# Kernel tuning notes

Measured on AMD Instinct MI355X. Metric: run time of the kernel, lower is better.

Reference implementation:

```python
import jax, jax.numpy as jnp
import numpy as np

T, F, H = 2048, 256, 384  # seq_len, input_size, hidden_size


def setup_inputs() -> dict:
    key = jax.random.key(0)
    ks = jax.random.split(key, 16)
    s = 1.0 / np.sqrt(F)
    d = {"x": jax.random.normal(ks[0], (T, F), jnp.float32)}
    names = ["q", "k", "v", "i", "f", "o"]
    for j, n in enumerate(names):
        d[f"W{n}"] = jax.random.uniform(ks[1 + j], (H, F), jnp.float32, -s, s)
        d[f"b{n}"] = jax.random.uniform(ks[7 + j], (H,), jnp.float32, -s, s)
    d["conv_w"] = jax.random.uniform(ks[13], (1, 1, 4), jnp.float32, -0.5, 0.5)
    d["conv_b"] = jax.random.uniform(ks[14], (1,), jnp.float32, -0.5, 0.5)
    return d


def _forward(x, Wq, bq, Wk, bk, Wv, bv, Wi, bi, Wf, bf, Wo, bo, conv_w, conv_b):
    # Conv1d(1->1, kernel=4, padding=(3,3)) along time, per input feature.
    xt = x.T[:, None, :]  # (F, 1, T)  feature axis acts as batch
    y = jax.lax.conv_general_dilated(xt, conv_w, (1,), [(3, 3)])  # (F, 1, T+3)
    xp = (y[:, 0, :] + conv_b[0]).T  # (T+3, F)

    inv_sqrt_h = 1.0 / jnp.sqrt(jnp.asarray(H, xp.dtype))
    # Precompute all per-step projections with dense GEMMs (time-parallel part).
    q = xp @ Wq.T + bq                      # (T+3, H)
    k = (xp @ Wk.T + bk) * inv_sqrt_h       # (T+3, H); extra bias_k is zero-init
    v = xp @ Wv.T + bv
    i = jnp.exp(xp @ Wi.T + bi)
    f = jax.nn.sigmoid(xp @ Wf.T + bf)
    o = jax.nn.sigmoid(xp @ Wo.T + bo)

    def step(carry, inp):
        C, n = carry                         # C: (H,H), n: (H,)
        qt, kt, vt, it, ft, ot = inp
        C = ft * C + it * jnp.outer(vt, kt)  # broadcast over last axis, as original
        n = ft * n + it * kt
        den = jnp.maximum(jnp.abs(jnp.dot(n, qt)), 1.0)
        h = ot * (C @ qt) / den
        return (C, n), h

    init = (jnp.zeros((H, H), xp.dtype), jnp.zeros((H,), xp.dtype))
    _, hs = jax.lax.scan(step, init, (q, k, v, i, f, o))
    return hs[-1]  # return_all=False -> last hidden state, shape (H,)


def reference(x, Wq, bq, Wk, bk, Wv, bv, Wi, bi, Wf, bf, Wo, bo, conv_w, conv_b):
    return _forward(x, Wq, bq, Wk, bk, Wv, bv, Wi, bi, Wf, bf, Wo, bo, conv_w, conv_b)
```

## Files before the change

kernel.cpp:

```cpp
#include <hip/hip_runtime.h>
#include <math.h>

#define T_IN 2048
#define TP   2051
#define F    256
#define H    384
#define BK   16
#define BT2  32
#define NT2  65
#define NCS  257
#define NC3  257

__device__ __forceinline__ float logsig(float z) {
    return (z >= 0.0f) ? -log1pf(__expf(-z)) : z - log1pf(__expf(z));
}

union F4 { float4 v; float f[4]; };

__global__ __launch_bounds__(256) void k1_front(const float* __restrict__ x,
        const float* __restrict__ cw, const float* __restrict__ cb,
        const float* __restrict__ Wq, const float* __restrict__ bq,
        const float* __restrict__ Wo, const float* __restrict__ bo,
        float* __restrict__ xp, float* __restrict__ q, float* __restrict__ o,
        float* __restrict__ zf) {
    int bid = blockIdx.x;
    int tid = threadIdx.x;
    if (bid < 513) {
        int t = bid * 4 + (tid >> 6);
        int f4 = tid & 63;
        if (t >= TP) return;
        float w[4] = {cw[0], cw[1], cw[2], cw[3]};
        float b = cb[0];
        float4 acc = {b, b, b, b};
        int i0 = t - 3;
        const float4* x4 = (const float4*)x;
        #pragma unroll
        for (int j = 0; j < 4; ++j) {
            int tt = i0 + j;
            if (tt >= 0 && tt < T_IN) {
                float4 xv = x4[tt * 64 + f4];
                acc.x = fmaf(w[j], xv.x, acc.x);
                acc.y = fmaf(w[j], xv.y, acc.y);
                acc.z = fmaf(w[j], xv.z, acc.z);
                acc.w = fmaf(w[j], xv.w, acc.w);
            }
        }
        ((float4*)xp)[t * 64 + f4] = acc;
    } else if (bid < 609) {
        int lane = tid & 63;
        int row = (bid - 513) * 4 + (tid >> 6);
        float w0 = cw[0], b = cb[0];
        float4 xr = ((const float4*)x)[2047 * 64 + lane];
        float4 xv;
        xv.x = fmaf(w0, xr.x, b);
        xv.y = fmaf(w0, xr.y, b);
        xv.z = fmaf(w0, xr.z, b);
        xv.w = fmaf(w0, xr.w, b);
        float4 q4 = *(const float4*)&Wq[row * 256 + lane * 4];
        float4 o4 = *(const float4*)&Wo[row * 256 + lane * 4];
        float aq = fmaf(xv.x, q4.x, fmaf(xv.y, q4.y, fmaf(xv.z, q4.z, xv.w * q4.w)));
        float ao = fmaf(xv.x, o4.x, fmaf(xv.y, o4.y, fmaf(xv.z, o4.z, xv.w * o4.w)));
        #pragma unroll
        for (int off = 32; off; off >>= 1) {
            aq += __shfl_down(aq, off, 64);
            ao += __shfl_down(ao, off, 64);
        }
        if (lane == 0) {
            q[row] = aq + bq[row];
            o[row] = 1.0f / (1.0f + __expf(-(ao + bo[row])));
        }
    } else {
        for (int i = tid; i < 272; i += 256) zf[i] = 0.0f;
    }
}

__global__ __launch_bounds__(256) void k2_proj(
    const float* __restrict__ xp,
    const float* __restrict__ Wk, const float* __restrict__ bk,
    const float* __restrict__ Wi, const float* __restrict__ bi,
    const float* __restrict__ Wf, const float* __restrict__ bf,
    float* __restrict__ zk, float* __restrict__ ai, float* __restrict__ lf,
    float* __restrict__ cs) {
    __shared__ float alds[2][BT2][20];
    __shared__ float wlds[2][BK][66];
    __shared__ float csred[8][66];
    int tid = threadIdx.x;
    int mz = blockIdx.z;
    const float* __restrict__ W    = (mz == 0) ? Wk : (mz == 1) ? Wi : Wf;
    const float* __restrict__ bias = (mz == 0) ? bk : (mz == 1) ? bi : bf;
    int t0 = blockIdx.x * BT2, b0 = blockIdx.y * 64;
    int tx = tid & 31, ty = tid >> 5;
    float2 acc[4];
    #pragma unroll
    for (int u = 0; u < 4; ++u) { acc[u].x = 0.f; acc[u].y = 0.f; }

    int wrow = tid >> 2;
    int wk4 = (tid & 3) * 4;
    int grow = (b0 + wrow) * 256 + wk4;
    int atq = tid >> 2;
    int arow = (t0 + atq) * 256 + wk4;
    bool aval = (tid < 128) && (t0 + atq < TP);

    float4 aw = {0.f, 0.f, 0.f, 0.f};
    float4 ww;
    if (aval) aw = *(const float4*)&xp[arow];
    ww = *(const float4*)&W[grow];

    for (int i = 0; i < 16; ++i) {
        int buf = i & 1;
        if (tid < 128) *(float4*)&alds[buf][atq][wk4] = aw;
        {
            F4 wu; wu.v = ww;
            #pragma unroll
            for (int j = 0; j < 4; ++j)
                wlds[buf][wk4 + j][wrow] = wu.f[j];
        }
        __syncthreads();
        if (i < 15) {
            int k0 = (i + 1) * BK;
            if (aval) aw = *(const float4*)&xp[arow + k0];
            ww = *(const float4*)&W[grow + k0];
        }
        #pragma unroll
        for (int g = 0; g < 4; ++g) {
            F4 av0, av1, av2, av3;
            av0.v = *(const float4*)&alds[buf][4 * ty + 0][4 * g];
            av1.v = *(const float4*)&alds[buf][4 * ty + 1][4 * g];
            av2.v = *(const float4*)&alds[buf][4 * ty + 2][4 * g];
            av3.v = *(const float4*)&alds[buf][4 * ty + 3][4 * g];
            #pragma unroll
            for (int j = 0; j < 4; ++j) {
                float2 w0 = *(const float2*)&wlds[buf][4 * g + j][2 * tx];
                acc[0].x = fmaf(av0.f[j], w0.x, acc[0].x);
                acc[0].y = fmaf(av0.f[j], w0.y, acc[0].y);
                acc[1].x = fmaf(av1.f[j], w0.x, acc[1].x);
                acc[1].y = fmaf(av1.f[j], w0.y, acc[1].y);
                acc[2].x = fmaf(av2.f[j], w0.x, acc[2].x);
                acc[2].y = fmaf(av2.f[j], w0.y, acc[2].y);
                acc[3].x = fmaf(av3.f[j], w0.x, acc[3].x);
                acc[3].y = fmaf(av3.f[j], w0.y, acc[3].y);
            }
        }
    }
    int bA = b0 + 2 * tx;
    float2 b2 = *(const float2*)&bias[bA];
    if (mz == 0) {
        const float sc = 0.05103103630798287f;
        #pragma unroll
        for (int u = 0; u < 4; ++u) {
            int t = t0 + 4 * ty + u;
            if (t < TP) {
                float2 v;
                v.x = (acc[u].x + b2.x) * sc; v.y = (acc[u].y + b2.y) * sc;
                *(float2*)&zk[t * H + bA] = v;
            }
        }
    } else if (mz == 1) {
        #pragma unroll
        for (int u = 0; u < 4; ++u) {
            int t = t0 + 4 * ty + u;
            if (t < TP) {
                float2 v;
                v.x = acc[u].x + b2.x; v.y = acc[u].y + b2.y;
                *(float2*)&ai[t * H + bA] = v;
            }
        }
    } else {
        float2 lsum = {0.f, 0.f};
        #pragma unroll
        for (int u = 0; u < 4; ++u) {
            int t = t0 + 4 * ty + u;
            if (t < TP) {
                float2 l2;
                l2.x = logsig(acc[u].x + b2.x);
                l2.y = logsig(acc[u].y + b2.y);
                *(float2*)&lf[t * H + bA] = l2;
                lsum.x += l2.x; lsum.y += l2.y;
            }
        }
        *(float2*)&csred[ty][2 * tx] = lsum;
        __syncthreads();
        int cl = tid >> 6;
        int bb = tid & 63;
        int c = blockIdx.x * 4 + cl;
        if (c < NCS)
            cs[c * H + b0 + bb] = csred[2 * cl][bb] + csred[2 * cl + 1][bb];
    }
}

__global__ __launch_bounds__(64) void k3b_scan(const float* __restrict__ cs,
                                               float* __restrict__ co) {
    int b = blockIdx.x * 64 + threadIdx.x;
    float L = 0.0f;
    #pragma unroll 16
    for (int c = NCS - 1; c >= 0; --c) {
        co[c * H + b] = L;
        L += cs[c * H + b];
    }
}

__global__ __launch_bounds__(384) void k3_fused(
    const float* __restrict__ ai, const float* __restrict__ lf,
    const float* __restrict__ zk, const float* __restrict__ co,
    const float* __restrict__ q, const float* __restrict__ xp,
    float* __restrict__ zf, float* __restrict__ Gf) {
    __shared__ float zred[6][256];
    __shared__ float gred[6];
    int tid = threadIdx.x;
    int w = tid >> 6, lane = tid & 63;
    int c = blockIdx.x, ts = c * 8;
    float co0 = co[c * H + tid];
    float qb = q[tid];
    float aiv[8], lfv[8], zkv[8];
    float4 xv[8];
    if (ts + 8 <= TP) {
        #pragma unroll
        for (int u = 0; u < 8; ++u) {
            int idx = (ts + u) * H + tid;
            aiv[u] = ai[idx]; lfv[u] = lf[idx]; zkv[u] = zk[idx];
            xv[u] = *(const float4*)&xp[(ts + u) * 256 + lane * 4];
        }
    } else {
        #pragma unroll
        for (int u = 0; u < 8; ++u) {
            if (ts + u < TP) {
                int idx = (ts + u) * H + tid;
                aiv[u] = ai[idx]; lfv[u] = lf[idx]; zkv[u] = zk[idx];
                xv[u] = *(const float4*)&xp[(ts + u) * 256 + lane * 4];
            } else {
                aiv[u] = -1e30f; lfv[u] = 0.f; zkv[u] = 0.f;
                xv[u].x = xv[u].y = xv[u].z = xv[u].w = 0.f;
            }
        }
    }
    float S = 0.f, gsum = 0.f;
    float z0 = 0.f, z1 = 0.f, z2 = 0.f, z3 = 0.f;
    #pragma unroll
    for (int u = 7; u >= 0; --u) {
        float wv = __expf(aiv[u] + co0 + S) * zkv[u] * qb;
        S += lfv[u];
        float s = wv;
        s += __shfl_xor(s, 1, 64);
        s += __shfl_xor(s, 2, 64);
        s += __shfl_xor(s, 4, 64);
        s += __shfl_xor(s, 8, 64);
        s += __shfl_xor(s, 16, 64);
        s += __shfl_xor(s, 32, 64);
        gsum += s;
        z0 = fmaf(s, xv[u].x, z0);
        z1 = fmaf(s, xv[u].y, z1);
        z2 = fmaf(s, xv[u].z, z2);
        z3 = fmaf(s, xv[u].w, z3);
    }
    zred[w][lane * 4 + 0] = z0;
    zred[w][lane * 4 + 1] = z1;
    zred[w][lane * 4 + 2] = z2;
    zred[w][lane * 4 + 3] = z3;
    if (lane == 0) gred[w] = gsum;
    __syncthreads();
    if (tid < 256) {
        float s = zred[0][tid] + zred[1][tid] + zred[2][tid]
                + zred[3][tid] + zred[4][tid] + zred[5][tid];
        atomicAdd(&zf[tid], s);
    }
    if (tid == 0)
        atomicAdd(Gf, gred[0] + gred[1] + gred[2] + gred[3] + gred[4] + gred[5]);
}

__global__ __launch_bounds__(256) void k6_out(const float* __restrict__ zf,
        const float* __restrict__ Gf,
        const float* __restrict__ Wv, const float* __restrict__ bv,
        const float* __restrict__ o, float* __restrict__ out) {
    int tid = threadIdx.x;
    int lane = tid & 63;
    int row = blockIdx.x * 4 + (tid >> 6);
    float Gv = Gf[0];
    float4 zv = *(const float4*)&zf[lane * 4];
    float4 wv = *(const float4*)&Wv[row * 256 + lane * 4];
    float acc = fmaf(zv.x, wv.x, fmaf(zv.y, wv.y, fmaf(zv.z, wv.z, zv.w * wv.w)));
    #pragma unroll
    for (int off = 32; off; off >>= 1) acc += __shfl_down(acc, off, 64);
    if (lane == 0)
        out[row] = o[row] * (acc + bv[row] * Gv) / fmaxf(fabsf(Gv), 1.0f);
}

extern "C" void kernel_launch(void* const* d_in, const int* in_sizes, int n_in,
                              void* d_out, int out_size, void* d_ws, size_t ws_size,
                              hipStream_t stream) {
    const float* x  = (const float*)d_in[0];
    const float* Wq = (const float*)d_in[1];  const float* bq = (const float*)d_in[2];
    const float* Wk = (const float*)d_in[3];  const float* bk = (const float*)d_in[4];
    const float* Wv = (const float*)d_in[5];  const float* bv = (const float*)d_in[6];
    const float* Wi = (const float*)d_in[7];  const float* bi = (const float*)d_in[8];
    const float* Wf = (const float*)d_in[9];  const float* bf = (const float*)d_in[10];
    const float* Wo = (const float*)d_in[11]; const float* bo = (const float*)d_in[12];
    const float* cw = (const float*)d_in[13]; const float* cb = (const float*)d_in[14];
    float* out = (float*)d_out;

    float* ws = (float*)d_ws;
    float* xp  = ws;
    float* zk  = xp  + TP * F;
    float* ai  = zk  + TP * H;
    float* lf  = ai  + TP * H;
    float* cs  = lf  + TP * H;
    float* co  = cs  + NCS * H;
    float* qv  = co  + NCS * H;
    float* ov  = qv  + H;
    float* zf  = ov  + H;
    float* Gf  = zf  + F;

    k1_front<<<610, 256, 0, stream>>>(x, cw, cb, Wq, bq, Wo, bo, xp, qv, ov, zf);
    k2_proj<<<dim3(NT2, 6, 3), 256, 0, stream>>>(xp, Wk, bk, Wi, bi, Wf, bf, zk, ai, lf, cs);
    k3b_scan<<<6, 64, 0, stream>>>(cs, co);
    k3_fused<<<NC3, 384, 0, stream>>>(ai, lf, zk, co, qv, xp, zf, Gf);
    k6_out<<<96, 256, 0, stream>>>(zf, Gf, Wv, bv, ov, out);
}
```

Before: 140.7 us.

## Transpose conv output and restructure projection GEMM with register-held weight rows

The conv front kernel now also writes a time-major-transposed copy of xp (padded stride, zero-filled tail) via a shared-memory transpose. The projection GEMM is rewritten to tile 64 timesteps by 32 outputs, with each wave loading 8 weight rows directly into registers as 8-float vectors and streaming transposed activations through double-buffered LDS. Results are staged through shared memory for coalesced row-major stores, and chunk sums for the forget-gate prefix are computed from the staged tile. This aims to cut LDS traffic and increase arithmetic per load, but it adds an extra transposed write in the front kernel and uses wave-uniform global weight loads.

```diff
diff --git a/kernel.cpp b/kernel.cpp
--- a/kernel.cpp
+++ b/kernel.cpp
@@ -5,47 +5,57 @@
 #define TP   2051
 #define F    256
 #define H    384
-#define BK   16
-#define BT2  32
-#define NT2  65
+#define XTS  2112
+#define NT4  33
+#define NBP  12
 #define NCS  257
 #define NC3  257
 
+typedef __attribute__((ext_vector_type(8))) float float8;
+
 __device__ __forceinline__ float logsig(float z) {
     return (z >= 0.0f) ? -log1pf(__expf(-z)) : z - log1pf(__expf(z));
 }
-
-union F4 { float4 v; float f[4]; };
 
 __global__ __launch_bounds__(256) void k1_front(const float* __restrict__ x,
         const float* __restrict__ cw, const float* __restrict__ cb,
         const float* __restrict__ Wq, const float* __restrict__ bq,
         const float* __restrict__ Wo, const float* __restrict__ bo,
-        float* __restrict__ xp, float* __restrict__ q, float* __restrict__ o,
+        float* __restrict__ xp, float* __restrict__ xpT,
+        float* __restrict__ q, float* __restrict__ o,
         float* __restrict__ zf) {
     int bid = blockIdx.x;
     int tid = threadIdx.x;
     if (bid < 513) {
-        int t = bid * 4 + (tid >> 6);
+        __shared__ float tr[4][257];
+        int tl = tid >> 6;
         int f4 = tid & 63;
-        if (t >= TP) return;
-        float w[4] = {cw[0], cw[1], cw[2], cw[3]};
-        float b = cb[0];
-        float4 acc = {b, b, b, b};
-        int i0 = t - 3;
-        const float4* x4 = (const float4*)x;
-        #pragma unroll
-        for (int j = 0; j < 4; ++j) {
-            int tt = i0 + j;
-            if (tt >= 0 && tt < T_IN) {
-                float4 xv = x4[tt * 64 + f4];
-                acc.x = fmaf(w[j], xv.x, acc.x);
-                acc.y = fmaf(w[j], xv.y, acc.y);
-                acc.z = fmaf(w[j], xv.z, acc.z);
-                acc.w = fmaf(w[j], xv.w, acc.w);
+        int t = bid * 4 + tl;
+        float4 acc = {0.f, 0.f, 0.f, 0.f};
+        if (t < TP) {
+            float w[4] = {cw[0], cw[1], cw[2], cw[3]};
+            float b = cb[0];
+            acc.x = b; acc.y = b; acc.z = b; acc.w = b;
+            int i0 = t - 3;
+            const float4* x4 = (const float4*)x;
+            #pragma unroll
+            for (int j = 0; j < 4; ++j) {
+                int tt = i0 + j;
+                if (tt >= 0 && tt < T_IN) {
+                    float4 xv = x4[tt * 64 + f4];
+                    acc.x = fmaf(w[j], xv.x, acc.x);
+                    acc.y = fmaf(w[j], xv.y, acc.y);
+                    acc.z = fmaf(w[j], xv.z, acc.z);
+                    acc.w = fmaf(w[j], xv.w, acc.w);
+                }
             }
-        }
-        ((float4*)xp)[t * 64 + f4] = acc;
+            ((float4*)xp)[t * 64 + f4] = acc;
+        }
+        *(float4*)&tr[tl][f4 * 4] = acc;
+        __syncthreads();
+        float4 v;
+        v.x = tr[0][tid]; v.y = tr[1][tid]; v.z = tr[2][tid]; v.w = tr[3][tid];
+        *(float4*)&xpT[tid * XTS + bid * 4] = v;
     } else if (bid < 609) {
         int lane = tid & 63;
         int row = (bid - 513) * 4 + (tid >> 6);
@@ -71,120 +81,104 @@
         }
     } else {
         for (int i = tid; i < 272; i += 256) zf[i] = 0.0f;
+        for (int i = tid; i < 256 * 60; i += 256) {
+            int r = i / 60, c = 2052 + i % 60;
+            xpT[r * XTS + c] = 0.0f;
+        }
     }
 }
 
 __global__ __launch_bounds__(256) void k2_proj(
-    const float* __restrict__ xp,
+    const float* __restrict__ xpT,
     const float* __restrict__ Wk, const float* __restrict__ bk,
     const float* __restrict__ Wi, const float* __restrict__ bi,
     const float* __restrict__ Wf, const float* __restrict__ bf,
     float* __restrict__ zk, float* __restrict__ ai, float* __restrict__ lf,
     float* __restrict__ cs) {
-    __shared__ float alds[2][BT2][20];
-    __shared__ float wlds[2][BK][66];
-    __shared__ float csred[8][66];
+    __shared__ float als[2][8][64];
+    __shared__ float st[32][65];
     int tid = threadIdx.x;
+    int lane = tid & 63;
+    int wv = __builtin_amdgcn_readfirstlane(tid >> 6);
     int mz = blockIdx.z;
     const float* __restrict__ W    = (mz == 0) ? Wk : (mz == 1) ? Wi : Wf;
     const float* __restrict__ bias = (mz == 0) ? bk : (mz == 1) ? bi : bf;
-    int t0 = blockIdx.x * BT2, b0 = blockIdx.y * 64;
-    int tx = tid & 31, ty = tid >> 5;
-    float2 acc[4];
+    int t0 = blockIdx.x * 64, p0 = blockIdx.y * 32;
+    const float* __restrict__ Wb = W + (p0 + wv * 8) * 256;
+
+    float acc[8];
     #pragma unroll
-    for (int u = 0; u < 4; ++u) { acc[u].x = 0.f; acc[u].y = 0.f; }
-
-    int wrow = tid >> 2;
-    int wk4 = (tid & 3) * 4;
-    int grow = (b0 + wrow) * 256 + wk4;
-    int atq = tid >> 2;
-    int arow = (t0 + atq) * 256 + wk4;
-    bool aval = (tid < 128) && (t0 + atq < TP);
-
-    float4 aw = {0.f, 0.f, 0.f, 0.f};
-    float4 ww;
-    if (aval) aw = *(const float4*)&xp[arow];
-    ww = *(const float4*)&W[grow];
-
-    for (int i = 0; i < 16; ++i) {
-        int buf = i & 1;
-        if (tid < 128) *(float4*)&alds[buf][atq][wk4] = aw;
-        {
-            F4 wu; wu.v = ww;
+    for (int r = 0; r < 8; ++r) acc[r] = 0.f;
+
+    int kr = tid >> 5;
+    int tq = (tid & 31) * 2;
+    const float* ap = &xpT[kr * XTS + t0 + tq];
+    float2 areg = *(const float2*)ap;
+
+    for (int kt = 0; kt < 32; ++kt) {
+        int buf = kt & 1;
+        *(float2*)&als[buf][kr][tq] = areg;
+        float8 wr0 = *(const float8*)&Wb[0 * 256 + kt * 8];
+        float8 wr1 = *(const float8*)&Wb[1 * 256 + kt * 8];
+        float8 wr2 = *(const float8*)&Wb[2 * 256 + kt * 8];
+        float8 wr3 = *(const float8*)&Wb[3 * 256 + kt * 8];
+        float8 wr4 = *(const float8*)&Wb[4 * 256 + kt * 8];
+        float8 wr5 = *(const float8*)&Wb[5 * 256 + kt * 8];
+        float8 wr6 = *(const float8*)&Wb[6 * 256 + kt * 8];
+        float8 wr7 = *(const float8*)&Wb[7 * 256 + kt * 8];
+        __syncthreads();
+        if (kt < 31) areg = *(const float2*)(ap + (kt + 1) * 8 * XTS);
+        #pragma unroll
+        for (int j = 0; j < 8; ++j) {
+            float a = als[buf][j][lane];
+            acc[0] = fmaf(wr0[j], a, acc[0]);
+            acc[1] = fmaf(wr1[j], a, acc[1]);
+            acc[2] = fmaf(wr2[j], a, acc[2]);
+            acc[3] = fmaf(wr3[j], a, acc[3]);
+            acc[4] = fmaf(wr4[j], a, acc[4]);
+            acc[5] = fmaf(wr5[j], a, acc[5]);
+            acc[6] = fmaf(wr6[j], a, acc[6]);
+            acc[7] = fmaf(wr7[j], a, acc[7]);
+        }
+    }
+    const float sc = 0.05103103630798287f;
+    __syncthreads();
+    #pragma unroll
+    for (int r = 0; r < 8; ++r) {
+        float v = acc[r] + bias[p0 + wv * 8 + r];
+        if (mz == 0) v *= sc;
+        else if (mz == 2) v = logsig(v);
+        st[wv * 8 + r][lane] = v;
+    }
+    __syncthreads();
+    float* __restrict__ OUT = (mz == 0) ? zk : (mz == 1) ? ai : lf;
+    {
+        int tloc = tid >> 2;
+        int bq = (tid & 3) * 8;
+        int t = t0 + tloc;
+        if (t < TP) {
+            float4 v0, v1;
+            v0.x = st[bq + 0][tloc]; v0.y = st[bq + 1][tloc];
+            v0.z = st[bq + 2][tloc]; v0.w = st[bq + 3][tloc];
+            v1.x = st[bq + 4][tloc]; v1.y = st[bq + 5][tloc];
+            v1.z = st[bq + 6][tloc]; v1.w = st[bq + 7][tloc];
+            *(float4*)&OUT[t * H + p0 + bq] = v0;
+            *(float4*)&OUT[t * H + p0 + bq + 4] = v1;
+        }
+    }
+    if (mz == 2) {
+        int b_l = tid & 31;
+        int ch = tid >> 5;
+        int c = blockIdx.x * 8 + ch;
+        if (c < NCS) {
+            float s = 0.f;
             #pragma unroll
-            for (int j = 0; j < 4; ++j)
-                wlds[buf][wk4 + j][wrow] = wu.f[j];
-        }
-        __syncthreads();
-        if (i < 15) {
-            int k0 = (i + 1) * BK;
-            if (aval) aw = *(const float4*)&xp[arow + k0];
-            ww = *(const float4*)&W[grow + k0];
-        }
-        #pragma unroll
-        for (int g = 0; g < 4; ++g) {
-            F4 av0, av1, av2, av3;
-            av0.v = *(const float4*)&alds[buf][4 * ty + 0][4 * g];
-            av1.v = *(const float4*)&alds[buf][4 * ty + 1][4 * g];
-            av2.v = *(const float4*)&alds[buf][4 * ty + 2][4 * g];
-            av3.v = *(const float4*)&alds[buf][4 * ty + 3][4 * g];
-            #pragma unroll
-            for (int j = 0; j < 4; ++j) {
-                float2 w0 = *(const float2*)&wlds[buf][4 * g + j][2 * tx];
-                acc[0].x = fmaf(av0.f[j], w0.x, acc[0].x);
-                acc[0].y = fmaf(av0.f[j], w0.y, acc[0].y);
-                acc[1].x = fmaf(av1.f[j], w0.x, acc[1].x);
-                acc[1].y = fmaf(av1.f[j], w0.y, acc[1].y);
-                acc[2].x = fmaf(av2.f[j], w0.x, acc[2].x);
-                acc[2].y = fmaf(av2.f[j], w0.y, acc[2].y);
-                acc[3].x = fmaf(av3.f[j], w0.x, acc[3].x);
-                acc[3].y = fmaf(av3.f[j], w0.y, acc[3].y);
+            for (int j = 0; j < 8; ++j) {
+                int t = t0 + ch * 8 + j;
+                if (t < TP) s += st[b_l][ch * 8 + j];
             }
-        }
-    }
-    int bA = b0 + 2 * tx;
-    float2 b2 = *(const float2*)&bias[bA];
-    if (mz == 0) {
-        const float sc = 0.05103103630798287f;
-        #pragma unroll
-        for (int u = 0; u < 4; ++u) {
-            int t = t0 + 4 * ty + u;
-            if (t < TP) {
-                float2 v;
-                v.x = (acc[u].x + b2.x) * sc; v.y = (acc[u].y + b2.y) * sc;
-                *(float2*)&zk[t * H + bA] = v;
-            }
-        }
-    } else if (mz == 1) {
-        #pragma unroll
-        for (int u = 0; u < 4; ++u) {
-            int t = t0 + 4 * ty + u;
-            if (t < TP) {
-                float2 v;
-                v.x = acc[u].x + b2.x; v.y = acc[u].y + b2.y;
-                *(float2*)&ai[t * H + bA] = v;
-            }
-        }
-    } else {
-        float2 lsum = {0.f, 0.f};
-        #pragma unroll
-        for (int u = 0; u < 4; ++u) {
-            int t = t0 + 4 * ty + u;
-            if (t < TP) {
-                float2 l2;
-                l2.x = logsig(acc[u].x + b2.x);
-                l2.y = logsig(acc[u].y + b2.y);
-                *(float2*)&lf[t * H + bA] = l2;
-                lsum.x += l2.x; lsum.y += l2.y;
-            }
-        }
-        *(float2*)&csred[ty][2 * tx] = lsum;
-        __syncthreads();
-        int cl = tid >> 6;
-        int bb = tid & 63;
-        int c = blockIdx.x * 4 + cl;
-        if (c < NCS)
-            cs[c * H + b0 + bb] = csred[2 * cl][bb] + csred[2 * cl + 1][bb];
+            cs[c * H + p0 + b_l] = s;
+        }
     }
 }
 
@@ -308,9 +302,10 @@
     float* ov  = qv  + H;
     float* zf  = ov  + H;
     float* Gf  = zf  + F;
-
-    k1_front<<<610, 256, 0, stream>>>(x, cw, cb, Wq, bq, Wo, bo, xp, qv, ov, zf);
-    k2_proj<<<dim3(NT2, 6, 3), 256, 0, stream>>>(xp, Wk, bk, Wi, bi, Wf, bf, zk, ai, lf, cs);
+    float* xpT = zf  + 512;
+
+    k1_front<<<610, 256, 0, stream>>>(x, cw, cb, Wq, bq, Wo, bo, xp, xpT, qv, ov, zf);
+    k2_proj<<<dim3(NT4, NBP, 3), 256, 0, stream>>>(xpT, Wk, bk, Wi, bi, Wf, bf, zk, ai, lf, cs);
     k3b_scan<<<6, 64, 0, stream>>>(cs, co);
     k3_fused<<<NC3, 384, 0, stream>>>(ai, lf, zk, co, qv, xp, zf, Gf);
     k6_out<<<96, 256, 0, stream>>>(zf, Gf, Wv, bv, ov, out);
```

Measured after the change: 150.2 us. +6.8%, slower.
